# Kernel tuning notes

Hardware: AMD Instinct MI355X
Metric: run time of the kernel (lower is better)

## Reference

```python
import jax, jax.numpy as jnp
import numpy as np
from jax import lax

H = 1024   # hidden_dim
C = 3      # output_dim
B = 128    # batch
T = 128    # seq len


def gru_scan(x_seq, h0, W_ih, W_hh, b_ih, b_hh):
    """Torch-equation GRU over x_seq: [T, B, H]; h0: [B, H]. Masks in the
    original forward are all-ones, so the mask_mult blending is identity and
    o_t == h_t for a single-layer unidirectional GRU."""
    gates_x = jnp.einsum('tbh,gh->tbg', x_seq, W_ih) + b_ih  # [T, B, 3H]

    def step(h, gx):
        gh = h @ W_hh.T + b_hh
        xr, xz, xn = jnp.split(gx, 3, axis=-1)
        hr, hz, hn = jnp.split(gh, 3, axis=-1)
        r = jax.nn.sigmoid(xr + hr)
        z = jax.nn.sigmoid(xz + hz)
        n = jnp.tanh(xn + r * hn)
        h_new = (1.0 - z) * n + z * h
        return h_new, h_new

    h_n, o_s = lax.scan(step, h0, gates_x)
    return o_s, h_n


def setup_inputs() -> dict:
    key = jax.random.key(0)
    ks = jax.random.split(key, 20)
    s = 1.0 / np.sqrt(H)
    u = lambda k, shape: jax.random.uniform(k, shape, jnp.float32, -s, s)
    inp = {
        'premise': jax.random.normal(ks[0], (B, T, H), jnp.float32),
        'hypothesis': jax.random.normal(ks[1], (B, T, H), jnp.float32),
        'p_Wih': u(ks[2], (3 * H, H)), 'p_Whh': u(ks[3], (3 * H, H)),
        'p_bih': u(ks[4], (3 * H,)), 'p_bhh': u(ks[5], (3 * H,)),
        'h_Wih': u(ks[6], (3 * H, H)), 'h_Whh': u(ks[7], (3 * H, H)),
        'h_bih': u(ks[8], (3 * H,)), 'h_bhh': u(ks[9], (3 * H,)),
        'W_y': jax.random.normal(ks[10], (H, H), jnp.float32) * 0.02,
        'W_h': jax.random.normal(ks[11], (H, H), jnp.float32) * 0.02,
        'W_alpha': jax.random.normal(ks[12], (H, 1), jnp.float32) * 0.02,
        'W_x': jax.random.normal(ks[13], (H, H), jnp.float32) * 0.02,
        'W_p': jax.random.normal(ks[14], (H, H), jnp.float32) * 0.02,
        'out_w': u(ks[15], (C, H)), 'out_b': u(ks[16], (C,)),
    }
    return inp


def reference(premise, hypothesis,
              p_Wih, p_Whh, p_bih, p_bhh,
              h_Wih, h_Whh, h_bih, h_bhh,
              W_y, W_h, W_alpha, W_x, W_p, out_w, out_b):
    batch = premise.shape[0]
    # dropout disabled (deterministic reference); masks are all ones.
    enc_p = jnp.transpose(premise, (1, 0, 2))     # [T, B, H]
    enc_h = jnp.transpose(hypothesis, (1, 0, 2))  # [T, B, H]
    h0 = jnp.zeros((batch, H), premise.dtype)

    o_p, h_n = gru_scan(enc_p, h0, p_Wih, p_Whh, p_bih, p_bhh)
    o_h, h_n = gru_scan(enc_h, h_n, h_Wih, h_Whh, h_bih, h_bhh)

    # Bahdanau-style attention over premise outputs using last hypothesis state
    h_last = o_h[-1]                               # [B, H]
    Y = jnp.transpose(o_p, (1, 0, 2))              # [B, T, H]
    Wy = jnp.einsum('bth,hd->btd', Y, W_y)         # [B, T, H]
    Wh = h_last @ W_h                              # [B, H]
    M = jnp.tanh(Wy + Wh[:, None, :])              # [B, T, H]
    scores = jnp.einsum('bth,ho->bt', M, W_alpha)  # [B, T]
    # mask is all ones -> -1000*(1-mask) == 0
    alpha = jax.nn.softmax(scores, axis=1)         # [B, T]
    r = jnp.einsum('bt,bth->bh', alpha, Y)         # [B, H]

    h_star = jnp.tanh(r @ W_p + h_last @ W_x)      # [B, H]
    logits = jnp.tanh(h_star @ out_w.T + out_b)    # [B, C]
    pred = jax.nn.log_softmax(logits, axis=1)
    return pred
```

## Files before the change

### kernel.cpp

```cpp
#include <hip/hip_runtime.h>

#define HD 1024
#define BB 128
#define TT 128

typedef short short8 __attribute__((ext_vector_type(8)));
typedef float f32x4 __attribute__((ext_vector_type(4)));
typedef unsigned short us4 __attribute__((ext_vector_type(4)));

#define MFMA(a, b, c) __builtin_amdgcn_mfma_f32_16x16x32_bf16((a), (b), (c), 0, 0, 0)

__device__ __forceinline__ float b2f(unsigned short u) {
  union { unsigned int i; float f; } v; v.i = ((unsigned int)u) << 16; return v.f;
}
__device__ __forceinline__ unsigned short f2b(float f) {
  union { float f; unsigned int i; } v; v.f = f;
  unsigned int i = v.i;
  return (unsigned short)((i + 0x7FFFu + ((i >> 16) & 1u)) >> 16);
}
__device__ __forceinline__ short8 ld8(const unsigned short* p) {
  return *reinterpret_cast<const short8*>(p);
}

struct DIn { const unsigned short* h; const float* f; };

__device__ __forceinline__ short8 ld8i(const DIn in, size_t idx, int isf) {
  if (isf) {
    const float4* p = (const float4*)(in.f + idx);
    float4 a = p[0], b = p[1];
    short8 r;
    r[0] = (short)f2b(a.x); r[1] = (short)f2b(a.y);
    r[2] = (short)f2b(a.z); r[3] = (short)f2b(a.w);
    r[4] = (short)f2b(b.x); r[5] = (short)f2b(b.y);
    r[6] = (short)f2b(b.z); r[7] = (short)f2b(b.w);
    return r;
  }
  return ld8(in.h + idx);
}
__device__ __forceinline__ float ld1i(const DIn in, size_t idx, int isf) {
  return isf ? in.f[idx] : b2f(in.h[idx]);
}
__device__ __forceinline__ short8 ld8_coh(const unsigned long long* q) {
  union { unsigned long long u[2]; short8 s; } v;
  v.u[0] = __hip_atomic_load((unsigned long long*)q,     __ATOMIC_RELAXED, __HIP_MEMORY_SCOPE_AGENT);
  v.u[1] = __hip_atomic_load((unsigned long long*)q + 1, __ATOMIC_RELAXED, __HIP_MEMORY_SCOPE_AGENT);
  return v.s;
}
__device__ __forceinline__ float sigm(float x) {
  x = fminf(fmaxf(x, -30.f), 30.f);
  return 1.0f / (1.0f + __expf(-x));
}
__device__ __forceinline__ float tanh_f(float x) {
  x = fminf(fmaxf(x, -15.f), 15.f);
  float e = __expf(2.0f * x);
  return (e - 1.0f) / (e + 1.0f);
}

__global__ __launch_bounds__(64) void probe_kernel(const unsigned char* p, int* flag) {
  int t = threadIdx.x;
  unsigned char b = p[t * 4 + 1] & 0x7F;
  int s = (b >= 0x34 && b <= 0x41) ? 1 : 0;
  s += __shfl_xor(s, 1);  s += __shfl_xor(s, 2);  s += __shfl_xor(s, 4);
  s += __shfl_xor(s, 8);  s += __shfl_xor(s, 16); s += __shfl_xor(s, 32);
  if (t == 0) *flag = (s > 32) ? 0 : 1;
}

__global__ __launch_bounds__(256) void conv_kernel(DIn in, unsigned short* out,
                                                   const int* flag) {
  const int isf = *flag;
  size_t i = ((size_t)blockIdx.x * 256 + threadIdx.x) * 8;
  *(short8*)(out + i) = ld8i(in, i, isf);
}

struct ScanParams {
  DIn prem, hyp;
  DIn pbih, pbhh, hbih, hbhh;
  const unsigned short *cWihP, *cWhhP, *cWihH, *cWhhH;
  unsigned short *hbuf;
  unsigned short *op;
  int *bar;
};

__global__ __launch_bounds__(256) void scan_kernel(ScanParams P) {
  const int tid = threadIdx.x;
  const int wv = tid >> 6;
  const int lane = tid & 63;
  const int quad = lane >> 4, l16 = lane & 15;
  const int bid = blockIdx.x;
  const int xcd = bid & 7;
  const int y = bid >> 3;
  const int jg = (xcd << 3) | (y & 7);
  const int bc = y >> 3;
  const int row0 = bc << 5;
  const int col0 = jg << 4;
  const int mem = bid & 63;
  const int isf = P.bar[992];

  __shared__ float s_gh[4][32][52];
  __shared__ float s_gx[4][32][52];
  __shared__ float s_h[32][16];

  const int er = tid >> 2;
  const int ec0 = (tid & 3) << 2;

  if (tid < 128)
    for (int q = 0; q < 4; ++q) s_h[er][ec0 + q] = 0.0f;

  float bir[4], biz[4], bin_[4], bhr[4], bhz[4], bhn[4];
  f32x4 gxa[2][3];
  const f32x4 zf = {0.f, 0.f, 0.f, 0.f};

  int* gflag = P.bar + 256 + (bc << 6);
  const int kk0 = wv << 3;

  {
#pragma unroll
    for (int mi = 0; mi < 2; ++mi)
#pragma unroll
      for (int gi = 0; gi < 3; ++gi) gxa[mi][gi] = zf;
    const size_t x0 = (size_t)(row0 + l16) * TT * HD;
    const size_t x1 = (size_t)(row0 + 16 + l16) * TT * HD;
#pragma unroll 2
    for (int kk = kk0; kk < kk0 + 8; ++kk) {
      int k = (kk << 5) + (quad << 3);
      short8 a0 = ld8i(P.prem, x0 + k, isf);
      short8 a1 = ld8i(P.prem, x1 + k, isf);
#pragma unroll
      for (int gi = 0; gi < 3; ++gi) {
        short8 b = ld8(P.cWihP + (size_t)((gi << 10) + col0 + l16) * HD + k);
        gxa[0][gi] = MFMA(a0, b, gxa[0][gi]);
        gxa[1][gi] = MFMA(a1, b, gxa[1][gi]);
      }
    }
  }

  for (int t = 0; t < 256; ++t) {
#pragma unroll
    for (int mi = 0; mi < 2; ++mi)
#pragma unroll
      for (int gi = 0; gi < 3; ++gi)
#pragma unroll
        for (int i = 0; i < 4; ++i)
          s_gx[wv][(mi << 4) + (quad << 2) + i][(gi << 4) + l16] = gxa[mi][gi][i];

    {
      f32x4 gha[2][3];
#pragma unroll
      for (int mi = 0; mi < 2; ++mi)
#pragma unroll
        for (int gi = 0; gi < 3; ++gi) gha[mi][gi] = zf;
      if (t > 0) {
        const unsigned long long* hq =
            (const unsigned long long*)P.hbuf + (((size_t)(t & 1) * (BB * HD)) >> 2);
        const unsigned short* W = (t < 128) ? P.cWhhP : P.cWhhH;
        const unsigned long long* q0 = hq + (((size_t)(row0 + l16) * HD) >> 2);
        const unsigned long long* q1 = hq + (((size_t)(row0 + 16 + l16) * HD) >> 2);
        short8 ha[8], hb[8];
#pragma unroll
        for (int u = 0; u < 8; ++u) {
          int k = ((kk0 + u) << 5) + (quad << 3);
          ha[u] = ld8_coh(q0 + (k >> 2));
          hb[u] = ld8_coh(q1 + (k >> 2));
        }
#pragma unroll
        for (int u = 0; u < 8; ++u) {
          int k = ((kk0 + u) << 5) + (quad << 3);
#pragma unroll
          for (int gi = 0; gi < 3; ++gi) {
            short8 b = ld8(W + (size_t)((gi << 10) + col0 + l16) * HD + k);
            gha[0][gi] = MFMA(ha[u], b, gha[0][gi]);
            gha[1][gi] = MFMA(hb[u], b, gha[1][gi]);
          }
        }
      }
#pragma unroll
      for (int mi = 0; mi < 2; ++mi)
#pragma unroll
        for (int gi = 0; gi < 3; ++gi)
#pragma unroll
          for (int i = 0; i < 4; ++i)
            s_gh[wv][(mi << 4) + (quad << 2) + i][(gi << 4) + l16] = gha[mi][gi][i];
    }
    __syncthreads();

    if ((t == 0 || t == 128) && tid < 128) {
      const DIn bih = (t < 128) ? P.pbih : P.hbih;
      const DIn bhh = (t < 128) ? P.pbhh : P.hbhh;
#pragma unroll
      for (int q = 0; q < 4; ++q) {
        int g = col0 + ec0 + q;
        bir[q] = ld1i(bih, g, isf);  biz[q] = ld1i(bih, 1024 + g, isf);
        bin_[q] = ld1i(bih, 2048 + g, isf);
        bhr[q] = ld1i(bhh, g, isf);  bhz[q] = ld1i(bhh, 1024 + g, isf);
        bhn[q] = ld1i(bhh, 2048 + g, isf);
      }
    }

    if (tid < 128) {
      unsigned short hout[4];
#pragma unroll
      for (int q = 0; q < 4; ++q) {
        int c = ec0 + q;
        float gxr = s_gx[0][er][c]      + s_gx[1][er][c]
                  + s_gx[2][er][c]      + s_gx[3][er][c];
        float gxz = s_gx[0][er][16 + c] + s_gx[1][er][16 + c]
                  + s_gx[2][er][16 + c] + s_gx[3][er][16 + c];
        float gxn = s_gx[0][er][32 + c] + s_gx[1][er][32 + c]
                  + s_gx[2][er][32 + c] + s_gx[3][er][32 + c];
        float ghr = s_gh[0][er][c]      + s_gh[1][er][c]
                  + s_gh[2][er][c]      + s_gh[3][er][c];
        float ghz = s_gh[0][er][16 + c] + s_gh[1][er][16 + c]
                  + s_gh[2][er][16 + c] + s_gh[3][er][16 + c];
        float ghn = s_gh[0][er][32 + c] + s_gh[1][er][32 + c]
                  + s_gh[2][er][32 + c] + s_gh[3][er][32 + c];
        float r = sigm(gxr + bir[q] + ghr + bhr[q]);
        float z = sigm(gxz + biz[q] + ghz + bhz[q]);
        float n = tanh_f(gxn + bin_[q] + r * (ghn + bhn[q]));
        float h = (1.0f - z) * n + z * s_h[er][c];
        s_h[er][c] = h;
        hout[q] = f2b(h);
      }
      union { us4 v; unsigned long long q; } pv;
      pv.v.x = hout[0]; pv.v.y = hout[1]; pv.v.z = hout[2]; pv.v.w = hout[3];
      int grow = row0 + er, gcol = col0 + ec0;
      size_t idx = ((size_t)((t + 1) & 1) * (BB * HD) + (size_t)grow * HD + gcol) >> 2;
      __hip_atomic_store((unsigned long long*)P.hbuf + idx, pv.q,
                         __ATOMIC_RELAXED, __HIP_MEMORY_SCOPE_AGENT);
      if (t < 128)
        *(us4*)(P.op + (size_t)t * (BB * HD) + (size_t)grow * HD + gcol) = pv.v;
    }
    __syncthreads();

    if (t == 255) break;

    if (tid == 0)
      __hip_atomic_store(gflag + mem, t + 1, __ATOMIC_RELAXED,
                         __HIP_MEMORY_SCOPE_AGENT);

    {
      int tn = t + 1;
      const DIn X = (tn < 128) ? P.prem : P.hyp;
      const unsigned short* Wi = (tn < 128) ? P.cWihP : P.cWihH;
      int tl = tn & 127;
#pragma unroll
      for (int mi = 0; mi < 2; ++mi)
#pragma unroll
        for (int gi = 0; gi < 3; ++gi) gxa[mi][gi] = zf;
      const size_t x0 = ((size_t)(row0 + l16) * TT + tl) * HD;
      const size_t x1 = ((size_t)(row0 + 16 + l16) * TT + tl) * HD;
#pragma unroll 2
      for (int kk = kk0; kk < kk0 + 8; ++kk) {
        int k = (kk << 5) + (quad << 3);
        short8 a0 = ld8i(X, x0 + k, isf);
        short8 a1 = ld8i(X, x1 + k, isf);
#pragma unroll
        for (int gi = 0; gi < 3; ++gi) {
          short8 b = ld8(Wi + (size_t)((gi << 10) + col0 + l16) * HD + k);
          gxa[0][gi] = MFMA(a0, b, gxa[0][gi]);
          gxa[1][gi] = MFMA(a1, b, gxa[1][gi]);
        }
      }
    }

    if (wv == 0) {
      for (;;) {
        int v = __hip_atomic_load(gflag + lane, __ATOMIC_RELAXED,
                                  __HIP_MEMORY_SCOPE_AGENT);
        if (__ballot(v >= t + 1) == ~0ull) break;
        __builtin_amdgcn_s_sleep(2);
      }
    }
    __syncthreads();
  }
}

__global__ __launch_bounds__(256) void transpose_kernel(DIn in, unsigned short* out,
                                                        const int* flag) {
  __shared__ unsigned short tile[64][65];
  const int isf = *flag;
  const int b = blockIdx.x;
  const int d0 = (b & 15) << 6, h0 = (b >> 4) << 6;
  const int c = threadIdx.x & 63, rg = threadIdx.x >> 6;
#pragma unroll
  for (int i = 0; i < 16; ++i) {
    int r = (rg << 4) + i;
    size_t idx = (size_t)(h0 + r) * HD + d0 + c;
    tile[r][c] = isf ? f2b(in.f[idx]) : in.h[idx];
  }
  __syncthreads();
#pragma unroll
  for (int i = 0; i < 16; ++i) {
    int r = (rg << 4) + i;
    out[(size_t)(d0 + r) * HD + h0 + c] = tile[c][r];
  }
}

__global__ __launch_bounds__(256) void wh_kernel(const unsigned short* A,
                                                 const unsigned short* Bt, float* out) {
  const int wvv = threadIdx.x >> 6, lane = threadIdx.x & 63;
  const int quad = lane >> 4, l16 = lane & 15;
  const int m0 = (blockIdx.x >> 3) * 64, n0 = (blockIdx.x & 7) * 128 + wvv * 32;
  const f32x4 zf = {0.f, 0.f, 0.f, 0.f};
  f32x4 acc[4][2];
#pragma unroll
  for (int mi = 0; mi < 4; ++mi) { acc[mi][0] = zf; acc[mi][1] = zf; }
  for (int kk = 0; kk < 32; ++kk) {
    int k = (kk << 5) + (quad << 3);
    short8 a[4], bb[2];
#pragma unroll
    for (int mi = 0; mi < 4; ++mi) a[mi] = ld8(A + (size_t)(m0 + mi * 16 + l16) * HD + k);
#pragma unroll
    for (int nt = 0; nt < 2; ++nt) bb[nt] = ld8(Bt + (size_t)(n0 + nt * 16 + l16) * HD + k);
#pragma unroll
    for (int mi = 0; mi < 4; ++mi)
#pragma unroll
      for (int nt = 0; nt < 2; ++nt) acc[mi][nt] = MFMA(a[mi], bb[nt], acc[mi][nt]);
  }
#pragma unroll
  for (int mi = 0; mi < 4; ++mi)
#pragma unroll
    for (int nt = 0; nt < 2; ++nt)
#pragma unroll
      for (int i = 0; i < 4; ++i)
        out[(size_t)(m0 + mi * 16 + quad * 4 + i) * HD + n0 + nt * 16 + l16] = acc[mi][nt][i];
}

__global__ __launch_bounds__(256) void score_kernel(const unsigned short* op,
                                                    const unsigned short* WyT,
                                                    const float* Wh,
                                                    DIn Walpha,
                                                    float* scores,
                                                    const int* flag) {
  const int isf = *flag;
  const int wvv = threadIdx.x >> 6, lane = threadIdx.x & 63;
  const int quad = lane >> 4, l16 = lane & 15;
  const int r0 = blockIdx.x * 64;
  __shared__ float ssc[4][64];
  float sp[4][4];
#pragma unroll
  for (int mi = 0; mi < 4; ++mi)
#pragma unroll
    for (int i = 0; i < 4; ++i) sp[mi][i] = 0.f;
  const f32x4 zf = {0.f, 0.f, 0.f, 0.f};

  for (int dc = 0; dc < 8; ++dc) {
    const int n0 = dc * 128 + wvv * 32;
    f32x4 acc[4][2];
#pragma unroll
    for (int mi = 0; mi < 4; ++mi) { acc[mi][0] = zf; acc[mi][1] = zf; }
    for (int kk = 0; kk < 32; ++kk) {
      int k = (kk << 5) + (quad << 3);
      short8 a[4], bb[2];
#pragma unroll
      for (int mi = 0; mi < 4; ++mi) a[mi] = ld8(op + (size_t)(r0 + mi * 16 + l16) * HD + k);
#pragma unroll
      for (int nt = 0; nt < 2; ++nt) bb[nt] = ld8(WyT + (size_t)(n0 + nt * 16 + l16) * HD + k);
#pragma unroll
      for (int mi = 0; mi < 4; ++mi)
#pragma unroll
        for (int nt = 0; nt < 2; ++nt) acc[mi][nt] = MFMA(a[mi], bb[nt], acc[mi][nt]);
    }
    float wa[2];
#pragma unroll
    for (int nt = 0; nt < 2; ++nt) wa[nt] = ld1i(Walpha, n0 + nt * 16 + l16, isf);
#pragma unroll
    for (int mi = 0; mi < 4; ++mi)
#pragma unroll
      for (int nt = 0; nt < 2; ++nt)
#pragma unroll
        for (int i = 0; i < 4; ++i) {
          int r = r0 + mi * 16 + quad * 4 + i;
          int bb2 = r & 127;
          int d = n0 + nt * 16 + l16;
          float v = tanh_f(acc[mi][nt][i] + Wh[(size_t)bb2 * HD + d]);
          sp[mi][i] += v * wa[nt];
        }
  }
#pragma unroll
  for (int mi = 0; mi < 4; ++mi)
#pragma unroll
    for (int i = 0; i < 4; ++i) {
      float v = sp[mi][i];
      v += __shfl_xor(v, 1); v += __shfl_xor(v, 2);
      v += __shfl_xor(v, 4); v += __shfl_xor(v, 8);
      sp[mi][i] = v;
    }
  if (l16 == 0) {
#pragma unroll
    for (int mi = 0; mi < 4; ++mi)
#pragma unroll
      for (int i = 0; i < 4; ++i) ssc[wvv][mi * 16 + quad * 4 + i] = sp[mi][i];
  }
  __syncthreads();
  if (threadIdx.x < 64)
    scores[r0 + threadIdx.x] =
        ssc[0][threadIdx.x] + ssc[1][threadIdx.x] + ssc[2][threadIdx.x] + ssc[3][threadIdx.x];
}

__global__ __launch_bounds__(256) void softrv_kernel(const float* scores,
                                                     const unsigned short* op,
                                                     unsigned short* rbf) {
  const int b = blockIdx.x;
  const int tid = threadIdx.x, wvv = tid >> 6, lane = tid & 63;
  __shared__ float sal[128];
  __shared__ float red[8];
  float sv = -3.0e38f;
  if (tid < 128) sv = scores[tid * BB + b];
  float m = sv;
  m = fmaxf(m, __shfl_xor(m, 1));  m = fmaxf(m, __shfl_xor(m, 2));
  m = fmaxf(m, __shfl_xor(m, 4));  m = fmaxf(m, __shfl_xor(m, 8));
  m = fmaxf(m, __shfl_xor(m, 16)); m = fmaxf(m, __shfl_xor(m, 32));
  if (lane == 0) red[wvv] = m;
  __syncthreads();
  float M = fmaxf(fmaxf(red[0], red[1]), fmaxf(red[2], red[3]));
  float e = (tid < 128) ? __expf(sv - M) : 0.0f;
  float s = e;
  s += __shfl_xor(s, 1);  s += __shfl_xor(s, 2);  s += __shfl_xor(s, 4);
  s += __shfl_xor(s, 8);  s += __shfl_xor(s, 16); s += __shfl_xor(s, 32);
  if (lane == 0) red[4 + wvv] = s;
  __syncthreads();
  float S = red[4] + red[5] + red[6] + red[7];
  if (tid < 128) sal[tid] = e / S;
  __syncthreads();
  float a0 = 0, a1 = 0, a2 = 0, a3 = 0;
  const unsigned short* base = op + (size_t)b * HD + tid * 4;
  for (int t2 = 0; t2 < 128; ++t2) {
    float w = sal[t2];
    us4 v = *(const us4*)(base + (size_t)t2 * (BB * HD));
    a0 += w * b2f(v.x); a1 += w * b2f(v.y); a2 += w * b2f(v.z); a3 += w * b2f(v.w);
  }
  us4 o; o.x = f2b(a0); o.y = f2b(a1); o.z = f2b(a2); o.w = f2b(a3);
  *(us4*)(rbf + (size_t)b * HD + tid * 4) = o;
}

__global__ __launch_bounds__(256) void hstar_kernel(const unsigned short* rbf,
                                                    const unsigned short* hlast,
                                                    const unsigned short* WpT,
                                                    const unsigned short* WxT,
                                                    unsigned short* hstar) {
  const int wvv = threadIdx.x >> 6, lane = threadIdx.x & 63;
  const int quad = lane >> 4, l16 = lane & 15;
  const int m0 = (blockIdx.x >> 3) * 64, n0 = (blockIdx.x & 7) * 128 + wvv * 32;
  const f32x4 zf = {0.f, 0.f, 0.f, 0.f};
  f32x4 acc[4][2];
#pragma unroll
  for (int mi = 0; mi < 4; ++mi) { acc[mi][0] = zf; acc[mi][1] = zf; }
  for (int kk = 0; kk < 64; ++kk) {
    int k = (kk << 5) + (quad << 3);
    const unsigned short* Ap; const unsigned short* Bp; int kl;
    if (kk < 32) { Ap = rbf;   Bp = WpT; kl = k; }
    else         { Ap = hlast; Bp = WxT; kl = k - 1024; }
    short8 a[4], bb[2];
#pragma unroll
    for (int mi = 0; mi < 4; ++mi) a[mi] = ld8(Ap + (size_t)(m0 + mi * 16 + l16) * HD + kl);
#pragma unroll
    for (int nt = 0; nt < 2; ++nt) bb[nt] = ld8(Bp + (size_t)(n0 + nt * 16 + l16) * HD + kl);
#pragma unroll
    for (int mi = 0; mi < 4; ++mi)
#pragma unroll
      for (int nt = 0; nt < 2; ++nt) acc[mi][nt] = MFMA(a[mi], bb[nt], acc[mi][nt]);
  }
#pragma unroll
  for (int mi = 0; mi < 4; ++mi)
#pragma unroll
    for (int nt = 0; nt < 2; ++nt)
#pragma unroll
      for (int i = 0; i < 4; ++i)
        hstar[(size_t)(m0 + mi * 16 + quad * 4 + i) * HD + n0 + nt * 16 + l16] =
            f2b(tanh_f(acc[mi][nt][i]));
}

__global__ __launch_bounds__(64) void out_kernel(const unsigned short* hstar,
                                                 DIn outw, DIn outb,
                                                 void* dout, const int* flag) {
  const int isf = *flag;
  const int b = blockIdx.x, lane = threadIdx.x;
  float l0 = 0, l1 = 0, l2 = 0;
  const short8* ph = (const short8*)(hstar + (size_t)b * HD + lane * 16);
  short8 h0 = ph[0], h1 = ph[1];
  for (int c = 0; c < 3; ++c) {
    short8 w0 = ld8i(outw, (size_t)c * HD + lane * 16, isf);
    short8 w1 = ld8i(outw, (size_t)c * HD + lane * 16 + 8, isf);
    float s = 0;
#pragma unroll
    for (int j = 0; j < 8; ++j)
      s += b2f((unsigned short)h0[j]) * b2f((unsigned short)w0[j]) +
           b2f((unsigned short)h1[j]) * b2f((unsigned short)w1[j]);
    s += __shfl_xor(s, 1);  s += __shfl_xor(s, 2);  s += __shfl_xor(s, 4);
    s += __shfl_xor(s, 8);  s += __shfl_xor(s, 16); s += __shfl_xor(s, 32);
    float v = tanh_f(s + ld1i(outb, c, isf));
    if (c == 0) l0 = v; else if (c == 1) l1 = v; else l2 = v;
  }
  float mx = fmaxf(l0, fmaxf(l1, l2));
  float lse = mx + logf(__expf(l0 - mx) + __expf(l1 - mx) + __expf(l2 - mx));
  if (lane < 3) {
    float v = ((lane == 0) ? l0 : (lane == 1) ? l1 : l2) - lse;
    if (isf) ((float*)dout)[b * 3 + lane] = v;
    else     ((unsigned short*)dout)[b * 3 + lane] = f2b(v);
  }
}

extern "C" void kernel_launch(void* const* d_in, const int* in_sizes, int n_in,
                              void* d_out, int out_size, void* d_ws, size_t ws_size,
                              hipStream_t stream) {
  DIn prem{(const unsigned short*)d_in[0],  (const float*)d_in[0]};
  DIn hyp {(const unsigned short*)d_in[1],  (const float*)d_in[1]};
  DIn pWih{(const unsigned short*)d_in[2],  (const float*)d_in[2]};
  DIn pWhh{(const unsigned short*)d_in[3],  (const float*)d_in[3]};
  DIn pbih{(const unsigned short*)d_in[4],  (const float*)d_in[4]};
  DIn pbhh{(const unsigned short*)d_in[5],  (const float*)d_in[5]};
  DIn hWih{(const unsigned short*)d_in[6],  (const float*)d_in[6]};
  DIn hWhh{(const unsigned short*)d_in[7],  (const float*)d_in[7]};
  DIn hbih{(const unsigned short*)d_in[8],  (const float*)d_in[8]};
  DIn hbhh{(const unsigned short*)d_in[9],  (const float*)d_in[9]};
  DIn Wy  {(const unsigned short*)d_in[10], (const float*)d_in[10]};
  DIn Whm {(const unsigned short*)d_in[11], (const float*)d_in[11]};
  DIn Wal {(const unsigned short*)d_in[12], (const float*)d_in[12]};
  DIn Wx  {(const unsigned short*)d_in[13], (const float*)d_in[13]};
  DIn Wp  {(const unsigned short*)d_in[14], (const float*)d_in[14]};
  DIn outw{(const unsigned short*)d_in[15], (const float*)d_in[15]};
  DIn outb{(const unsigned short*)d_in[16], (const float*)d_in[16]};

  char* ws = (char*)d_ws;
  int*            bar   = (int*)ws;
  unsigned short* hbuf  = (unsigned short*)(ws + 4096);
  float*          WhRes = (float*)(ws + 528384);
  float*          scr   = (float*)(ws + 1052672);
  unsigned short* rbf   = (unsigned short*)(ws + 1118208);
  unsigned short* hstar = (unsigned short*)(ws + 1380352);
  unsigned short* tb0   = (unsigned short*)(ws + 2097152);
  unsigned short* tb1   = (unsigned short*)(ws + 4194304);
  unsigned short* op    = (unsigned short*)(ws + 6291456);
  unsigned short* cWihP = (unsigned short*)(ws + 39845888);
  unsigned short* cWhhP = (unsigned short*)(ws + 46137344);
  unsigned short* cWihH = (unsigned short*)(ws + 52428800);
  unsigned short* cWhhH = (unsigned short*)(ws + 58720256);

  hipMemsetAsync(d_ws, 0, 4096, stream);
  hipLaunchKernelGGL(probe_kernel, dim3(1), dim3(64), 0, stream,
                     (const unsigned char*)d_in[0], bar + 992);

  hipLaunchKernelGGL(conv_kernel, dim3(1536), dim3(256), 0, stream, pWih, cWihP, bar + 992);
  hipLaunchKernelGGL(conv_kernel, dim3(1536), dim3(256), 0, stream, pWhh, cWhhP, bar + 992);
  hipLaunchKernelGGL(conv_kernel, dim3(1536), dim3(256), 0, stream, hWih, cWihH, bar + 992);
  hipLaunchKernelGGL(conv_kernel, dim3(1536), dim3(256), 0, stream, hWhh, cWhhH, bar + 992);

  ScanParams sp{prem, hyp, pbih, pbhh, hbih, hbhh,
                cWihP, cWhhP, cWihH, cWhhH, hbuf, op, bar};
  hipLaunchKernelGGL(scan_kernel, dim3(256), dim3(256), 0, stream, sp);

  hipLaunchKernelGGL(transpose_kernel, dim3(256), dim3(256), 0, stream, Whm, tb0, bar + 992);
  hipLaunchKernelGGL(wh_kernel, dim3(16), dim3(256), 0, stream, hbuf, tb0, WhRes);

  hipLaunchKernelGGL(transpose_kernel, dim3(256), dim3(256), 0, stream, Wy, tb0, bar + 992);
  hipLaunchKernelGGL(score_kernel, dim3(256), dim3(256), 0, stream, op, tb0, WhRes,
                     Wal, scr, bar + 992);
  hipLaunchKernelGGL(softrv_kernel, dim3(128), dim3(256), 0, stream, scr, op, rbf);

  hipLaunchKernelGGL(transpose_kernel, dim3(256), dim3(256), 0, stream, Wp, tb0, bar + 992);
  hipLaunchKernelGGL(transpose_kernel, dim3(256), dim3(256), 0, stream, Wx, tb1, bar + 992);
  hipLaunchKernelGGL(hstar_kernel, dim3(16), dim3(256), 0, stream, rbf, hbuf, tb0, tb1, hstar);

  hipLaunchKernelGGL(out_kernel, dim3(128), dim3(64), 0, stream, hstar, outw, outb,
                     d_out, bar + 992);
}
```

Measured before the change: 5.637 ms.

## Cache recurrent W_hh slice in swizzled LDS and rebalance input-projection work across waves

Each block now stages its 48-row W_hh slice (96 KB bf16) into dynamic shared memory with an XOR swizzle, once per GRU direction. The recurrent MFMA loop then reads weights from LDS instead of global/L2 on every timestep. The hidden-state loads are issued earlier so they overlap the gate-score stores. The next-step input projection is split unevenly so the polling wave 0 does little of it, and the spin-wait sleep is shortened. The cost is about 150 KB of LDS per block, which limits occupancy to one block per CU, plus a reload stall at the layer switch.

New measurement: 5.871 ms. +4.1%, slower.

```diff
diff --git a/kernel.cpp b/kernel.cpp
--- a/kernel.cpp
+++ b/kernel.cpp
@@ -81,11 +81,26 @@
   int *bar;
 };
 
+__device__ __forceinline__ void stage_w(unsigned int* sW, const unsigned short* W,
+                                        int col0, int tid) {
+  const unsigned int* Wu = (const unsigned int*)W;
+#pragma unroll 4
+  for (int it = 0; it < 96; ++it) {
+    int idx = (it << 8) + tid;
+    int r = idx >> 9, dw = idx & 511;
+    int gi = r >> 4, c = r & 15;
+    unsigned int v = Wu[((size_t)((gi << 10) + col0 + c) << 9) + dw];
+    sW[(r << 9) + ((((dw >> 2) ^ (r & 7)) << 2) | (dw & 3))] = v;
+  }
+}
+
 __global__ __launch_bounds__(256) void scan_kernel(ScanParams P) {
+  extern __shared__ unsigned int sW[];
   const int tid = threadIdx.x;
   const int wv = tid >> 6;
   const int lane = tid & 63;
   const int quad = lane >> 4, l16 = lane & 15;
+  const int rl = l16 & 7;
   const int bid = blockIdx.x;
   const int xcd = bid & 7;
   const int y = bid >> 3;
@@ -112,6 +127,8 @@
 
   int* gflag = P.bar + 256 + (bc << 6);
   const int kk0 = wv << 3;
+  const int gxs = wv ? (10 * wv - 8) : 0;
+  const int gxe = wv ? (10 * wv + 2) : 2;
 
   {
 #pragma unroll
@@ -121,7 +138,7 @@
     const size_t x0 = (size_t)(row0 + l16) * TT * HD;
     const size_t x1 = (size_t)(row0 + 16 + l16) * TT * HD;
 #pragma unroll 2
-    for (int kk = kk0; kk < kk0 + 8; ++kk) {
+    for (int kk = gxs; kk < gxe; ++kk) {
       int k = (kk << 5) + (quad << 3);
       short8 a0 = ld8i(P.prem, x0 + k, isf);
       short8 a1 = ld8i(P.prem, x1 + k, isf);
@@ -133,8 +150,29 @@
       }
     }
   }
+  stage_w(sW, P.cWhhP, col0, tid);
+  __syncthreads();
 
   for (int t = 0; t < 256; ++t) {
+    if (t == 128) {
+      stage_w(sW, P.cWhhH, col0, tid);
+      __syncthreads();
+    }
+
+    short8 ha[8], hb[8];
+    if (t > 0) {
+      const unsigned long long* hq =
+          (const unsigned long long*)P.hbuf + (((size_t)(t & 1) * (BB * HD)) >> 2);
+      const unsigned long long* q0 = hq + (((size_t)(row0 + l16) * HD) >> 2);
+      const unsigned long long* q1 = hq + (((size_t)(row0 + 16 + l16) * HD) >> 2);
+#pragma unroll
+      for (int u = 0; u < 8; ++u) {
+        int k = ((kk0 + u) << 5) + (quad << 3);
+        ha[u] = ld8_coh(q0 + (k >> 2));
+        hb[u] = ld8_coh(q1 + (k >> 2));
+      }
+    }
+
 #pragma unroll
     for (int mi = 0; mi < 2; ++mi)
 #pragma unroll
@@ -150,24 +188,13 @@
 #pragma unroll
         for (int gi = 0; gi < 3; ++gi) gha[mi][gi] = zf;
       if (t > 0) {
-        const unsigned long long* hq =
-            (const unsigned long long*)P.hbuf + (((size_t)(t & 1) * (BB * HD)) >> 2);
-        const unsigned short* W = (t < 128) ? P.cWhhP : P.cWhhH;
-        const unsigned long long* q0 = hq + (((size_t)(row0 + l16) * HD) >> 2);
-        const unsigned long long* q1 = hq + (((size_t)(row0 + 16 + l16) * HD) >> 2);
-        short8 ha[8], hb[8];
 #pragma unroll
         for (int u = 0; u < 8; ++u) {
-          int k = ((kk0 + u) << 5) + (quad << 3);
-          ha[u] = ld8_coh(q0 + (k >> 2));
-          hb[u] = ld8_coh(q1 + (k >> 2));
-        }
-#pragma unroll
-        for (int u = 0; u < 8; ++u) {
-          int k = ((kk0 + u) << 5) + (quad << 3);
+          int g = ((kk0 + u) << 2) + quad;
 #pragma unroll
           for (int gi = 0; gi < 3; ++gi) {
-            short8 b = ld8(W + (size_t)((gi << 10) + col0 + l16) * HD + k);
+            int r = (gi << 4) + l16;
+            short8 b = *(const short8*)(sW + (r << 9) + ((g ^ rl) << 2));
             gha[0][gi] = MFMA(ha[u], b, gha[0][gi]);
             gha[1][gi] = MFMA(hb[u], b, gha[1][gi]);
           }
@@ -249,7 +276,7 @@
       const size_t x0 = ((size_t)(row0 + l16) * TT + tl) * HD;
       const size_t x1 = ((size_t)(row0 + 16 + l16) * TT + tl) * HD;
 #pragma unroll 2
-      for (int kk = kk0; kk < kk0 + 8; ++kk) {
+      for (int kk = gxs; kk < gxe; ++kk) {
         int k = (kk << 5) + (quad << 3);
         short8 a0 = ld8i(X, x0 + k, isf);
         short8 a1 = ld8i(X, x1 + k, isf);
@@ -267,7 +294,7 @@
         int v = __hip_atomic_load(gflag + lane, __ATOMIC_RELAXED,
                                   __HIP_MEMORY_SCOPE_AGENT);
         if (__ballot(v >= t + 1) == ~0ull) break;
-        __builtin_amdgcn_s_sleep(2);
+        __builtin_amdgcn_s_sleep(1);
       }
     }
     __syncthreads();
@@ -536,6 +563,13 @@
   unsigned short* cWihH = (unsigned short*)(ws + 52428800);
   unsigned short* cWhhH = (unsigned short*)(ws + 58720256);
 
+  static int attr_done = 0;
+  if (!attr_done) {
+    hipFuncSetAttribute((const void*)scan_kernel,
+                        hipFuncAttributeMaxDynamicSharedMemorySize, 98304);
+    attr_done = 1;
+  }
+
   hipMemsetAsync(d_ws, 0, 4096, stream);
   hipLaunchKernelGGL(probe_kernel, dim3(1), dim3(64), 0, stream,
                      (const unsigned char*)d_in[0], bar + 992);
@@ -547,7 +581,7 @@
 
   ScanParams sp{prem, hyp, pbih, pbhh, hbih, hbhh,
                 cWihP, cWhhP, cWihH, cWhhH, hbuf, op, bar};
-  hipLaunchKernelGGL(scan_kernel, dim3(256), dim3(256), 0, stream, sp);
+  hipLaunchKernelGGL(scan_kernel, dim3(256), dim3(256), 98304, stream, sp);
 
   hipLaunchKernelGGL(transpose_kernel, dim3(256), dim3(256), 0, stream, Whm, tb0, bar + 992);
   hipLaunchKernelGGL(wh_kernel, dim3(16), dim3(256), 0, stream, hbuf, tb0, WhRes);
```

## Use write-once hidden-state slots and rebalance input projection across waves

Applied to the files above, without the earlier changes.

When the workspace is large enough, each timestep's hidden state goes to its own slot instead of a double buffer. Reads can then use plain cached loads instead of coherent loads, and the separate output copy is dropped because downstream kernels read premise outputs straight from the slots. The h loads are issued before the gx LDS stores so their latency overlaps. The input-projection k-range is split unevenly so wave 0 does less gx work, and the spin-wait sleep is shortened. This costs more workspace, and correctness depends on no stale cached lines existing for freshly written slots.

After: 5.670 ms. About the same (+0.6%).

```diff
diff --git a/kernel.cpp b/kernel.cpp
--- a/kernel.cpp
+++ b/kernel.cpp
@@ -79,6 +79,7 @@
   unsigned short *hbuf;
   unsigned short *op;
   int *bar;
+  int wonce;
 };
 
 __global__ __launch_bounds__(256) void scan_kernel(ScanParams P) {
@@ -95,6 +96,7 @@
   const int col0 = jg << 4;
   const int mem = bid & 63;
   const int isf = P.bar[992];
+  const int wonce = P.wonce;
 
   __shared__ float s_gh[4][32][52];
   __shared__ float s_gx[4][32][52];
@@ -112,6 +114,8 @@
 
   int* gflag = P.bar + 256 + (bc << 6);
   const int kk0 = wv << 3;
+  const int gxs = wv ? (10 * wv - 8) : 0;
+  const int gxe = wv ? (10 * wv + 2) : 2;
 
   {
 #pragma unroll
@@ -121,7 +125,7 @@
     const size_t x0 = (size_t)(row0 + l16) * TT * HD;
     const size_t x1 = (size_t)(row0 + 16 + l16) * TT * HD;
 #pragma unroll 2
-    for (int kk = kk0; kk < kk0 + 8; ++kk) {
+    for (int kk = gxs; kk < gxe; ++kk) {
       int k = (kk << 5) + (quad << 3);
       short8 a0 = ld8i(P.prem, x0 + k, isf);
       short8 a1 = ld8i(P.prem, x1 + k, isf);
@@ -133,35 +137,51 @@
       }
     }
   }
+  __syncthreads();
 
   for (int t = 0; t < 256; ++t) {
-#pragma unroll
-    for (int mi = 0; mi < 2; ++mi)
-#pragma unroll
-      for (int gi = 0; gi < 3; ++gi)
-#pragma unroll
-        for (int i = 0; i < 4; ++i)
-          s_gx[wv][(mi << 4) + (quad << 2) + i][(gi << 4) + l16] = gxa[mi][gi][i];
-
-    {
-      f32x4 gha[2][3];
-#pragma unroll
-      for (int mi = 0; mi < 2; ++mi)
-#pragma unroll
-        for (int gi = 0; gi < 3; ++gi) gha[mi][gi] = zf;
-      if (t > 0) {
+    short8 ha[8], hb[8];
+    if (t > 0) {
+      if (wonce) {
+        const unsigned short* hs = P.hbuf + (size_t)t * (BB * HD);
+        const unsigned short* p0 = hs + (size_t)(row0 + l16) * HD;
+        const unsigned short* p1 = hs + (size_t)(row0 + 16 + l16) * HD;
+#pragma unroll
+        for (int u = 0; u < 8; ++u) {
+          int k = ((kk0 + u) << 5) + (quad << 3);
+          ha[u] = ld8(p0 + k);
+          hb[u] = ld8(p1 + k);
+        }
+      } else {
         const unsigned long long* hq =
             (const unsigned long long*)P.hbuf + (((size_t)(t & 1) * (BB * HD)) >> 2);
-        const unsigned short* W = (t < 128) ? P.cWhhP : P.cWhhH;
         const unsigned long long* q0 = hq + (((size_t)(row0 + l16) * HD) >> 2);
         const unsigned long long* q1 = hq + (((size_t)(row0 + 16 + l16) * HD) >> 2);
-        short8 ha[8], hb[8];
 #pragma unroll
         for (int u = 0; u < 8; ++u) {
           int k = ((kk0 + u) << 5) + (quad << 3);
           ha[u] = ld8_coh(q0 + (k >> 2));
           hb[u] = ld8_coh(q1 + (k >> 2));
         }
+      }
+    }
+
+#pragma unroll
+    for (int mi = 0; mi < 2; ++mi)
+#pragma unroll
+      for (int gi = 0; gi < 3; ++gi)
+#pragma unroll
+        for (int i = 0; i < 4; ++i)
+          s_gx[wv][(mi << 4) + (quad << 2) + i][(gi << 4) + l16] = gxa[mi][gi][i];
+
+    {
+      f32x4 gha[2][3];
+#pragma unroll
+      for (int mi = 0; mi < 2; ++mi)
+#pragma unroll
+        for (int gi = 0; gi < 3; ++gi) gha[mi][gi] = zf;
+      if (t > 0) {
+        const unsigned short* W = (t < 128) ? P.cWhhP : P.cWhhH;
 #pragma unroll
         for (int u = 0; u < 8; ++u) {
           int k = ((kk0 + u) << 5) + (quad << 3);
@@ -223,10 +243,11 @@
       union { us4 v; unsigned long long q; } pv;
       pv.v.x = hout[0]; pv.v.y = hout[1]; pv.v.z = hout[2]; pv.v.w = hout[3];
       int grow = row0 + er, gcol = col0 + ec0;
-      size_t idx = ((size_t)((t + 1) & 1) * (BB * HD) + (size_t)grow * HD + gcol) >> 2;
+      size_t slot = wonce ? (size_t)(t + 1) : (size_t)((t + 1) & 1);
+      size_t idx = (slot * (BB * HD) + (size_t)grow * HD + gcol) >> 2;
       __hip_atomic_store((unsigned long long*)P.hbuf + idx, pv.q,
                          __ATOMIC_RELAXED, __HIP_MEMORY_SCOPE_AGENT);
-      if (t < 128)
+      if (!wonce && t < 128)
         *(us4*)(P.op + (size_t)t * (BB * HD) + (size_t)grow * HD + gcol) = pv.v;
     }
     __syncthreads();
@@ -249,7 +270,7 @@
       const size_t x0 = ((size_t)(row0 + l16) * TT + tl) * HD;
       const size_t x1 = ((size_t)(row0 + 16 + l16) * TT + tl) * HD;
 #pragma unroll 2
-      for (int kk = kk0; kk < kk0 + 8; ++kk) {
+      for (int kk = gxs; kk < gxe; ++kk) {
         int k = (kk << 5) + (quad << 3);
         short8 a0 = ld8i(X, x0 + k, isf);
         short8 a1 = ld8i(X, x1 + k, isf);
@@ -267,7 +288,7 @@
         int v = __hip_atomic_load(gflag + lane, __ATOMIC_RELAXED,
                                   __HIP_MEMORY_SCOPE_AGENT);
         if (__ballot(v >= t + 1) == ~0ull) break;
-        __builtin_amdgcn_s_sleep(2);
+        __builtin_amdgcn_s_sleep(1);
       }
     }
     __syncthreads();
@@ -522,19 +543,48 @@
   DIn outb{(const unsigned short*)d_in[16], (const float*)d_in[16]};
 
   char* ws = (char*)d_ws;
-  int*            bar   = (int*)ws;
-  unsigned short* hbuf  = (unsigned short*)(ws + 4096);
-  float*          WhRes = (float*)(ws + 528384);
-  float*          scr   = (float*)(ws + 1052672);
-  unsigned short* rbf   = (unsigned short*)(ws + 1118208);
-  unsigned short* hstar = (unsigned short*)(ws + 1380352);
-  unsigned short* tb0   = (unsigned short*)(ws + 2097152);
-  unsigned short* tb1   = (unsigned short*)(ws + 4194304);
-  unsigned short* op    = (unsigned short*)(ws + 6291456);
-  unsigned short* cWihP = (unsigned short*)(ws + 39845888);
-  unsigned short* cWhhP = (unsigned short*)(ws + 46137344);
-  unsigned short* cWihH = (unsigned short*)(ws + 52428800);
-  unsigned short* cWhhH = (unsigned short*)(ws + 58720256);
+  const size_t SLOT = (size_t)BB * HD * 2;
+  const size_t NEED_WONCE = 4096 + 257 * SLOT + 524288 + 65536 + 262144 +
+                            262144 + 2 * 2097152 + 4 * 6291456;
+  int wonce = (ws_size >= NEED_WONCE) ? 1 : 0;
+
+  int* bar = (int*)ws;
+  unsigned short *hbuf, *opw, *opr, *hlast, *rbf, *hstar, *tb0, *tb1;
+  unsigned short *cWihP, *cWhhP, *cWihH, *cWhhH;
+  float *WhRes, *scr;
+
+  if (wonce) {
+    size_t o = 4096;
+    hbuf  = (unsigned short*)(ws + o);  o += 257 * SLOT;
+    WhRes = (float*)(ws + o);           o += 524288;
+    scr   = (float*)(ws + o);           o += 65536;
+    rbf   = (unsigned short*)(ws + o);  o += 262144;
+    hstar = (unsigned short*)(ws + o);  o += 262144;
+    tb0   = (unsigned short*)(ws + o);  o += 2097152;
+    tb1   = (unsigned short*)(ws + o);  o += 2097152;
+    cWihP = (unsigned short*)(ws + o);  o += 6291456;
+    cWhhP = (unsigned short*)(ws + o);  o += 6291456;
+    cWihH = (unsigned short*)(ws + o);  o += 6291456;
+    cWhhH = (unsigned short*)(ws + o);  o += 6291456;
+    opw   = nullptr;
+    opr   = hbuf + (size_t)BB * HD;
+    hlast = hbuf + 256 * (size_t)BB * HD;
+  } else {
+    hbuf  = (unsigned short*)(ws + 4096);
+    WhRes = (float*)(ws + 528384);
+    scr   = (float*)(ws + 1052672);
+    rbf   = (unsigned short*)(ws + 1118208);
+    hstar = (unsigned short*)(ws + 1380352);
+    tb0   = (unsigned short*)(ws + 2097152);
+    tb1   = (unsigned short*)(ws + 4194304);
+    opw   = (unsigned short*)(ws + 6291456);
+    opr   = opw;
+    cWihP = (unsigned short*)(ws + 39845888);
+    cWhhP = (unsigned short*)(ws + 46137344);
+    cWihH = (unsigned short*)(ws + 52428800);
+    cWhhH = (unsigned short*)(ws + 58720256);
+    hlast = hbuf;
+  }
 
   hipMemsetAsync(d_ws, 0, 4096, stream);
   hipLaunchKernelGGL(probe_kernel, dim3(1), dim3(64), 0, stream,
@@ -546,20 +596,20 @@
   hipLaunchKernelGGL(conv_kernel, dim3(1536), dim3(256), 0, stream, hWhh, cWhhH, bar + 992);
 
   ScanParams sp{prem, hyp, pbih, pbhh, hbih, hbhh,
-                cWihP, cWhhP, cWihH, cWhhH, hbuf, op, bar};
+                cWihP, cWhhP, cWihH, cWhhH, hbuf, opw, bar, wonce};
   hipLaunchKernelGGL(scan_kernel, dim3(256), dim3(256), 0, stream, sp);
 
   hipLaunchKernelGGL(transpose_kernel, dim3(256), dim3(256), 0, stream, Whm, tb0, bar + 992);
-  hipLaunchKernelGGL(wh_kernel, dim3(16), dim3(256), 0, stream, hbuf, tb0, WhRes);
+  hipLaunchKernelGGL(wh_kernel, dim3(16), dim3(256), 0, stream, hlast, tb0, WhRes);
 
   hipLaunchKernelGGL(transpose_kernel, dim3(256), dim3(256), 0, stream, Wy, tb0, bar + 992);
-  hipLaunchKernelGGL(score_kernel, dim3(256), dim3(256), 0, stream, op, tb0, WhRes,
+  hipLaunchKernelGGL(score_kernel, dim3(256), dim3(256), 0, stream, opr, tb0, WhRes,
                      Wal, scr, bar + 992);
-  hipLaunchKernelGGL(softrv_kernel, dim3(128), dim3(256), 0, stream, scr, op, rbf);
+  hipLaunchKernelGGL(softrv_kernel, dim3(128), dim3(256), 0, stream, scr, opr, rbf);
 
   hipLaunchKernelGGL(transpose_kernel, dim3(256), dim3(256), 0, stream, Wp, tb0, bar + 992);
   hipLaunchKernelGGL(transpose_kernel, dim3(256), dim3(256), 0, stream, Wx, tb1, bar + 992);
-  hipLaunchKernelGGL(hstar_kernel, dim3(16), dim3(256), 0, stream, rbf, hbuf, tb0, tb1, hstar);
+  hipLaunchKernelGGL(hstar_kernel, dim3(16), dim3(256), 0, stream, rbf, hlast, tb0, tb1, hstar);
 
   hipLaunchKernelGGL(out_kernel, dim3(128), dim3(64), 0, stream, hstar, outw, outb,
                      d_out, bar + 992);
```
